# Kernel tuning notes

Measured on AMD Instinct MI355X. Metric: run time of the kernel, lower is better.

The kernel has to match this reference:

```python
import jax, jax.numpy as jnp
import numpy as np

H = 128  # hidden_dim

def setup_inputs() -> dict:
    key = jax.random.key(0)
    ks = jax.random.split(key, 8)
    B, S = 32, 512
    return {
        "CNN_output": jax.random.normal(ks[0], (B, 4 * S, H), jnp.float32),
        "gaz_input": jax.random.normal(ks[1], (B, S, 128), jnp.float32),
        "gaz_input_back": jax.random.normal(ks[2], (B, S, 128), jnp.float32),
        "global_matrix": jax.random.normal(ks[3], (B, S, H), jnp.float32),
        "exper_input": jax.random.normal(ks[4], (B, S, H), jnp.float32),
        "W_cat": jax.random.normal(ks[5], (3 * H, 16 * H), jnp.float32) * (1.0 / np.sqrt(3 * H)),
        "b_cat": jnp.zeros((16 * H,), jnp.float32),
        "W_exp": jax.random.normal(ks[6], (H, 12 * H), jnp.float32) * (1.0 / np.sqrt(H)),
        "b_exp": jnp.zeros((12 * H,), jnp.float32),
    }


def _diag_gather(y, B, S, width):
    # y: [B, 4*S, 4*width]; for seq-block j pick columns j*width:(j+1)*width
    y = y.reshape(B, 4, S, 4, width)
    j = jnp.arange(4)
    y = y[:, j, :, j, :]              # [4, B, S, width]
    return jnp.transpose(y, (1, 0, 2, 3)).reshape(B, 4 * S, width)


def reference(CNN_output, gaz_input, gaz_input_back, global_matrix, exper_input,
              W_cat, b_cat, W_exp, b_exp):
    B, S4, _ = CNN_output.shape
    S = S4 // 4
    gaz = jnp.concatenate([gaz_input, gaz_input_back, gaz_input, gaz_input_back], axis=1)
    gm = jnp.tile(global_matrix, (1, 4, 1))
    exp_rep = jnp.tile(exper_input, (1, 4, 1))
    cat_in = jnp.concatenate([CNN_output, gaz, gm], axis=2)      # [B, 4S, 3H]
    cat_gates = _diag_gather(cat_in @ W_cat + b_cat, B, S, 4 * H)  # [B, 4S, 4H]
    exper_gates = _diag_gather(exp_rep @ W_exp + b_exp, B, S, 3 * H)  # [B, 4S, 3H]
    new_state = jnp.tanh(cat_gates[:, :, :H])
    gates = jax.nn.sigmoid(cat_gates[:, :, H:] + exper_gates)
    gates = jax.nn.softmax(gates.reshape(B, S4, 3, H), axis=2)
    state_cat = jnp.stack([new_state, CNN_output, exp_rep], axis=2)  # [B, 4S, 3, H]
    layer_output = jnp.sum(gates * state_cat, axis=2)                # [B, 4S, H]
    return tuple(layer_output[:, i * S:(i + 1) * S] for i in range(4))
```

## Files before the change

kernel.cpp:

```cpp
#include <hip/hip_runtime.h>

typedef unsigned short u16;
typedef unsigned int u32;
typedef short bf16x8 __attribute__((ext_vector_type(8)));
typedef float f32x4 __attribute__((ext_vector_type(4)));

#define HH 128

__device__ __forceinline__ u16 f2bf(float f) {
  u32 u = __float_as_uint(f);
  u += 0x7fffu + ((u >> 16) & 1u);
  return (u16)(u >> 16);
}
__device__ __forceinline__ u32 pack2(float a, float b) {
  return (u32)f2bf(a) | ((u32)f2bf(b) << 16);
}

__device__ __forceinline__ void lds_dma16(const void* g, void* l) {
  __builtin_amdgcn_global_load_lds(
      (const __attribute__((address_space(1))) u32*)g,
      (__attribute__((address_space(3))) u32*)l, 16, 0, 0);
}

__global__ void prep_w(const float* __restrict__ Wcat,
                       const float* __restrict__ Wexp, u16* __restrict__ Wc) {
  int tid = blockIdx.x * 256 + threadIdx.x;
  int p = tid & 3;
  int n = (tid >> 2) & 511;
  int kc = (tid >> 11) & 15;
  int q = tid >> 15;
  int lq = p ^ (n & 3) ^ ((n >> 2) & 3);
  int k0 = kc * 32 + lq * 8;
  float v[8];
#pragma unroll
  for (int j = 0; j < 8; ++j) {
    int k = k0 + j;
    v[j] = (k < 384) ? Wcat[k * 2048 + q * 512 + n]
                     : ((n < 128) ? 0.f : Wexp[(k - 384) * 1536 + q * 384 + (n - 128)]);
  }
  uint4 pk;
  pk.x = pack2(v[0], v[1]);
  pk.y = pack2(v[2], v[3]);
  pk.z = pack2(v[4], v[5]);
  pk.w = pack2(v[6], v[7]);
  ((uint4*)Wc)[tid] = pk;
}

__global__ __launch_bounds__(256, 2) void fused_gate(
    const float* __restrict__ CNN, const float* __restrict__ gaz,
    const float* __restrict__ gazb, const float* __restrict__ gm,
    const float* __restrict__ exper, const u16* __restrict__ Wc,
    const float* __restrict__ bcat, const float* __restrict__ bexp,
    float* __restrict__ out) {
  __shared__ u16 Abuf[64 * 32];
  __shared__ u16 Wbuf[512 * 32];

  const int tid = threadIdx.x;
  const int bx = blockIdx.x;
  const int tile = bx & 7;
  const int grp = bx >> 3;
  const int b = grp >> 2;
  const int q = grp & 3;
  const int s_base = tile * 64;
  const int lane = tid & 63;
  const int wave = tid >> 6;
  const int l15 = lane & 15;
  const int quad = lane >> 4;
  const int physq = quad ^ (lane & 3) ^ ((lane >> 2) & 3);

  const int arow = tid >> 2;
  const int ap = tid & 3;
  const int alq = ap ^ (arow & 3) ^ ((arow >> 2) & 3);
  const int srow = s_base + arow;
  const float* s0 = CNN + (size_t)(b * 2048 + q * 512 + srow) * HH;
  const float* s1 = ((q & 1) ? gazb : gaz) + (size_t)(b * 512 + srow) * HH;
  const float* s2 = gm + (size_t)(b * 512 + srow) * HH;
  const float* s3 = exper + (size_t)(b * 512 + srow) * HH;

  const u16* wsrc = Wc + (size_t)q * 16 * 512 * 32;

  f32x4 acc[4][4][2];
#pragma unroll
  for (int rt = 0; rt < 4; ++rt)
#pragma unroll
    for (int gg = 0; gg < 4; ++gg)
#pragma unroll
      for (int u = 0; u < 2; ++u) acc[rt][gg][u] = (f32x4)0.f;

  for (int kc = 0; kc < 16; ++kc) {
    const int k0 = kc * 32 + alq * 8;
    const int sel = k0 >> 7;
    const float* sp = (sel == 0) ? s0 : (sel == 1) ? s1 : (sel == 2) ? s2 : s3;
    sp += (k0 & 127);
    float4 f0 = *(const float4*)sp;
    float4 f1 = *(const float4*)(sp + 4);
    uint4 pk;
    pk.x = pack2(f0.x, f0.y);
    pk.y = pack2(f0.z, f0.w);
    pk.z = pack2(f1.x, f1.y);
    pk.w = pack2(f1.z, f1.w);
    *(uint4*)&Abuf[arow * 32 + ap * 8] = pk;

    const u16* wchunk = wsrc + (size_t)kc * 512 * 32;
#pragma unroll
    for (int i = 0; i < 8; ++i)
      lds_dma16(wchunk + i * 2048 + wave * 512 + lane * 8,
                &Wbuf[i * 2048 + wave * 512]);
    __syncthreads();

    bf16x8 af[4];
#pragma unroll
    for (int rt = 0; rt < 4; ++rt)
      af[rt] = *(const bf16x8*)&Abuf[(rt * 16 + l15) * 32 + physq * 8];
    bf16x8 bfr[4][2];
#pragma unroll
    for (int gg = 0; gg < 4; ++gg)
#pragma unroll
      for (int u = 0; u < 2; ++u) {
        const int n = gg * 128 + wave * 32 + u * 16 + l15;
        bfr[gg][u] = *(const bf16x8*)&Wbuf[n * 32 + physq * 8];
      }
#pragma unroll
    for (int rt = 0; rt < 4; ++rt)
#pragma unroll
      for (int gg = 0; gg < 4; ++gg)
#pragma unroll
        for (int u = 0; u < 2; ++u)
          acc[rt][gg][u] = __builtin_amdgcn_mfma_f32_16x16x32_bf16(
              af[rt], bfr[gg][u], acc[rt][gg][u], 0, 0, 0);
    __syncthreads();
  }

  const float* bcq = bcat + q * 512;
  const float* beq = bexp + q * 384;
  const size_t cnnbase = (size_t)(b * 2048 + q * 512 + s_base) * HH;
  const size_t expbase = (size_t)(b * 512 + s_base) * HH;
  const size_t outbase = (size_t)((q * 32 + b) * 512 + s_base) * HH;
#pragma unroll
  for (int u = 0; u < 2; ++u) {
    const int h = wave * 32 + u * 16 + l15;
    const float bc0 = bcq[h];
    const float bc1 = bcq[128 + h];
    const float bc2 = bcq[256 + h];
    const float bc3 = bcq[384 + h];
    const float be1 = beq[h];
    const float be2 = beq[128 + h];
    const float be3 = beq[256 + h];
#pragma unroll
    for (int rt = 0; rt < 4; ++rt) {
#pragma unroll
      for (int r = 0; r < 4; ++r) {
        const int row = rt * 16 + quad * 4 + r;
        const float c0 = acc[rt][0][u][r] + bc0;
        const float p1 = acc[rt][1][u][r] + bc1 + be1;
        const float p2 = acc[rt][2][u][r] + bc2 + be2;
        const float p3 = acc[rt][3][u][r] + bc3 + be3;
        const float e2c = __expf(2.f * c0);
        const float ns = 1.f - 2.f * __builtin_amdgcn_rcpf(e2c + 1.f);
        const float g1 = __builtin_amdgcn_rcpf(1.f + __expf(-p1));
        const float g2 = __builtin_amdgcn_rcpf(1.f + __expf(-p2));
        const float g3 = __builtin_amdgcn_rcpf(1.f + __expf(-p3));
        const float e1 = __expf(g1);
        const float e2 = __expf(g2);
        const float e3 = __expf(g3);
        const float inv = __builtin_amdgcn_rcpf(e1 + e2 + e3);
        const float cnn = CNN[cnnbase + (size_t)row * HH + h];
        const float ex = exper[expbase + (size_t)row * HH + h];
        out[outbase + (size_t)row * HH + h] = (e1 * ns + e2 * cnn + e3 * ex) * inv;
      }
    }
  }
}

extern "C" void kernel_launch(void* const* d_in, const int* in_sizes, int n_in,
                              void* d_out, int out_size, void* d_ws, size_t ws_size,
                              hipStream_t stream) {
  const float* CNN = (const float*)d_in[0];
  const float* gaz = (const float*)d_in[1];
  const float* gazb = (const float*)d_in[2];
  const float* gm = (const float*)d_in[3];
  const float* exper = (const float*)d_in[4];
  const float* Wcat = (const float*)d_in[5];
  const float* bcat = (const float*)d_in[6];
  const float* Wexp = (const float*)d_in[7];
  const float* bexp = (const float*)d_in[8];
  u16* Wc = (u16*)d_ws;

  prep_w<<<512, 256, 0, stream>>>(Wcat, Wexp, Wc);
  fused_gate<<<1024, 256, 0, stream>>>(CNN, gaz, gazb, gm, exper, Wc, bcat,
                                       bexp, (float*)d_out);
}
```

Measured before the change: 168.8 us.

## Split gate GEMM across hidden halves and coalesce weight prep via LDS transpose

The fused gate kernel now splits each 64-row tile into two blocks, each covering half of the hidden columns. This halves the LDS weight buffer and the accumulator registers, doubles the grid, and raises the launch-bounds occupancy target from 2 to 3. The weight-prep kernel now reads rows with vectorized loads and transposes them through shared memory, replacing the earlier strided scalar gathers. The cost is that each activation tile is loaded and converted to bf16 twice, once per half.

New measurement: 174.8 us. +3.5%, slower.

```diff
diff --git a/kernel.cpp b/kernel.cpp
--- a/kernel.cpp
+++ b/kernel.cpp
@@ -22,51 +22,83 @@
       (__attribute__((address_space(3))) u32*)l, 16, 0, 0);
 }
 
-__global__ void prep_w(const float* __restrict__ Wcat,
-                       const float* __restrict__ Wexp, u16* __restrict__ Wc) {
-  int tid = blockIdx.x * 256 + threadIdx.x;
-  int p = tid & 3;
-  int n = (tid >> 2) & 511;
-  int kc = (tid >> 11) & 15;
-  int q = tid >> 15;
-  int lq = p ^ (n & 3) ^ ((n >> 2) & 3);
-  int k0 = kc * 32 + lq * 8;
+__global__ __launch_bounds__(256) void prep_w(const float* __restrict__ Wcat,
+                                              const float* __restrict__ Wexp,
+                                              u16* __restrict__ Wc) {
+  const int bx = blockIdx.x;
+  const int nt = bx & 7;
+  const int kc = (bx >> 3) & 15;
+  const int q = bx >> 7;
+  __shared__ u16 T[32 * 72];
+
+  const int tid = threadIdx.x;
+  const int r = tid >> 3;
+  const int c8 = (tid & 7) * 8;
   float v[8];
-#pragma unroll
-  for (int j = 0; j < 8; ++j) {
-    int k = k0 + j;
-    v[j] = (k < 384) ? Wcat[k * 2048 + q * 512 + n]
-                     : ((n < 128) ? 0.f : Wexp[(k - 384) * 1536 + q * 384 + (n - 128)]);
+  if (kc < 12) {
+    const float* src =
+        Wcat + (size_t)(kc * 32 + r) * 2048 + q * 512 + nt * 64 + c8;
+    float4 a = *(const float4*)src;
+    float4 b = *(const float4*)(src + 4);
+    v[0] = a.x; v[1] = a.y; v[2] = a.z; v[3] = a.w;
+    v[4] = b.x; v[5] = b.y; v[6] = b.z; v[7] = b.w;
+  } else if (nt >= 2) {
+    const float* src = Wexp + (size_t)((kc - 12) * 32 + r) * 1536 + q * 384 +
+                       nt * 64 + c8 - 128;
+    float4 a = *(const float4*)src;
+    float4 b = *(const float4*)(src + 4);
+    v[0] = a.x; v[1] = a.y; v[2] = a.z; v[3] = a.w;
+    v[4] = b.x; v[5] = b.y; v[6] = b.z; v[7] = b.w;
+  } else {
+#pragma unroll
+    for (int j = 0; j < 8; ++j) v[j] = 0.f;
   }
   uint4 pk;
   pk.x = pack2(v[0], v[1]);
   pk.y = pack2(v[2], v[3]);
   pk.z = pack2(v[4], v[5]);
   pk.w = pack2(v[6], v[7]);
-  ((uint4*)Wc)[tid] = pk;
-}
-
-__global__ __launch_bounds__(256, 2) void fused_gate(
+  *(uint4*)&T[r * 72 + c8] = pk;
+  __syncthreads();
+
+  const int p = tid & 3;
+  const int nl = tid >> 2;
+  const int lq = p ^ (nl & 3) ^ ((nl >> 2) & 3);
+  u16 w[8];
+#pragma unroll
+  for (int j = 0; j < 8; ++j) w[j] = T[(lq * 8 + j) * 72 + nl];
+  uint4 o;
+  o.x = (u32)w[0] | ((u32)w[1] << 16);
+  o.y = (u32)w[2] | ((u32)w[3] << 16);
+  o.z = (u32)w[4] | ((u32)w[5] << 16);
+  o.w = (u32)w[6] | ((u32)w[7] << 16);
+  const size_t idx = ((size_t)((q * 16 + kc) * 512) + nt * 64 + nl) * 4 + p;
+  ((uint4*)Wc)[idx] = o;
+}
+
+__global__ __launch_bounds__(256, 3) void fused_gate(
     const float* __restrict__ CNN, const float* __restrict__ gaz,
     const float* __restrict__ gazb, const float* __restrict__ gm,
     const float* __restrict__ exper, const u16* __restrict__ Wc,
     const float* __restrict__ bcat, const float* __restrict__ bexp,
     float* __restrict__ out) {
   __shared__ u16 Abuf[64 * 32];
-  __shared__ u16 Wbuf[512 * 32];
+  __shared__ u16 Wbuf[256 * 32];
 
   const int tid = threadIdx.x;
   const int bx = blockIdx.x;
-  const int tile = bx & 7;
-  const int grp = bx >> 3;
+  const int half = bx & 1;
+  const int tile = (bx >> 1) & 7;
+  const int grp = bx >> 4;
   const int b = grp >> 2;
   const int q = grp & 3;
   const int s_base = tile * 64;
+  const int h0 = half * 64;
   const int lane = tid & 63;
   const int wave = tid >> 6;
   const int l15 = lane & 15;
   const int quad = lane >> 4;
-  const int physq = quad ^ (lane & 3) ^ ((lane >> 2) & 3);
+  const int physq = quad ^ (l15 & 3) ^ ((l15 >> 2) & 3);
 
   const int arow = tid >> 2;
   const int ap = tid & 3;
@@ -79,13 +111,11 @@
 
   const u16* wsrc = Wc + (size_t)q * 16 * 512 * 32;
 
-  f32x4 acc[4][4][2];
+  f32x4 acc[4][4];
 #pragma unroll
   for (int rt = 0; rt < 4; ++rt)
 #pragma unroll
-    for (int gg = 0; gg < 4; ++gg)
-#pragma unroll
-      for (int u = 0; u < 2; ++u) acc[rt][gg][u] = (f32x4)0.f;
+    for (int gg = 0; gg < 4; ++gg) acc[rt][gg] = (f32x4)0.f;
 
   for (int kc = 0; kc < 16; ++kc) {
     const int k0 = kc * 32 + alq * 8;
@@ -103,31 +133,29 @@
 
     const u16* wchunk = wsrc + (size_t)kc * 512 * 32;
 #pragma unroll
-    for (int i = 0; i < 8; ++i)
-      lds_dma16(wchunk + i * 2048 + wave * 512 + lane * 8,
-                &Wbuf[i * 2048 + wave * 512]);
+    for (int i = 0; i < 4; ++i) {
+      const int n0 = wave * 128 + h0 + i * 16;
+      lds_dma16(wchunk + (size_t)n0 * 32 + lane * 8,
+                &Wbuf[(wave * 64 + i * 16) * 32]);
+    }
     __syncthreads();
 
     bf16x8 af[4];
 #pragma unroll
     for (int rt = 0; rt < 4; ++rt)
       af[rt] = *(const bf16x8*)&Abuf[(rt * 16 + l15) * 32 + physq * 8];
-    bf16x8 bfr[4][2];
-#pragma unroll
-    for (int gg = 0; gg < 4; ++gg)
-#pragma unroll
-      for (int u = 0; u < 2; ++u) {
-        const int n = gg * 128 + wave * 32 + u * 16 + l15;
-        bfr[gg][u] = *(const bf16x8*)&Wbuf[n * 32 + physq * 8];
-      }
+    bf16x8 bfr[4];
+#pragma unroll
+    for (int gg = 0; gg < 4; ++gg) {
+      const int c = gg * 64 + wave * 16 + l15;
+      bfr[gg] = *(const bf16x8*)&Wbuf[c * 32 + physq * 8];
+    }
 #pragma unroll
     for (int rt = 0; rt < 4; ++rt)
 #pragma unroll
       for (int gg = 0; gg < 4; ++gg)
-#pragma unroll
-        for (int u = 0; u < 2; ++u)
-          acc[rt][gg][u] = __builtin_amdgcn_mfma_f32_16x16x32_bf16(
-              af[rt], bfr[gg][u], acc[rt][gg][u], 0, 0, 0);
+        acc[rt][gg] = __builtin_amdgcn_mfma_f32_16x16x32_bf16(
+            af[rt], bfr[gg], acc[rt][gg], 0, 0, 0);
     __syncthreads();
   }
 
@@ -136,38 +164,35 @@
   const size_t cnnbase = (size_t)(b * 2048 + q * 512 + s_base) * HH;
   const size_t expbase = (size_t)(b * 512 + s_base) * HH;
   const size_t outbase = (size_t)((q * 32 + b) * 512 + s_base) * HH;
-#pragma unroll
-  for (int u = 0; u < 2; ++u) {
-    const int h = wave * 32 + u * 16 + l15;
-    const float bc0 = bcq[h];
-    const float bc1 = bcq[128 + h];
-    const float bc2 = bcq[256 + h];
-    const float bc3 = bcq[384 + h];
-    const float be1 = beq[h];
-    const float be2 = beq[128 + h];
-    const float be3 = beq[256 + h];
-#pragma unroll
-    for (int rt = 0; rt < 4; ++rt) {
-#pragma unroll
-      for (int r = 0; r < 4; ++r) {
-        const int row = rt * 16 + quad * 4 + r;
-        const float c0 = acc[rt][0][u][r] + bc0;
-        const float p1 = acc[rt][1][u][r] + bc1 + be1;
-        const float p2 = acc[rt][2][u][r] + bc2 + be2;
-        const float p3 = acc[rt][3][u][r] + bc3 + be3;
-        const float e2c = __expf(2.f * c0);
-        const float ns = 1.f - 2.f * __builtin_amdgcn_rcpf(e2c + 1.f);
-        const float g1 = __builtin_amdgcn_rcpf(1.f + __expf(-p1));
-        const float g2 = __builtin_amdgcn_rcpf(1.f + __expf(-p2));
-        const float g3 = __builtin_amdgcn_rcpf(1.f + __expf(-p3));
-        const float e1 = __expf(g1);
-        const float e2 = __expf(g2);
-        const float e3 = __expf(g3);
-        const float inv = __builtin_amdgcn_rcpf(e1 + e2 + e3);
-        const float cnn = CNN[cnnbase + (size_t)row * HH + h];
-        const float ex = exper[expbase + (size_t)row * HH + h];
-        out[outbase + (size_t)row * HH + h] = (e1 * ns + e2 * cnn + e3 * ex) * inv;
-      }
+  const int h = h0 + wave * 16 + l15;
+  const float bc0 = bcq[h];
+  const float bc1 = bcq[128 + h];
+  const float bc2 = bcq[256 + h];
+  const float bc3 = bcq[384 + h];
+  const float be1 = beq[h];
+  const float be2 = beq[128 + h];
+  const float be3 = beq[256 + h];
+#pragma unroll
+  for (int rt = 0; rt < 4; ++rt) {
+#pragma unroll
+    for (int r = 0; r < 4; ++r) {
+      const int row = rt * 16 + quad * 4 + r;
+      const float c0 = acc[rt][0][r] + bc0;
+      const float p1 = acc[rt][1][r] + bc1 + be1;
+      const float p2 = acc[rt][2][r] + bc2 + be2;
+      const float p3 = acc[rt][3][r] + bc3 + be3;
+      const float e2c = __expf(2.f * c0);
+      const float ns = 1.f - 2.f * __builtin_amdgcn_rcpf(e2c + 1.f);
+      const float g1 = __builtin_amdgcn_rcpf(1.f + __expf(-p1));
+      const float g2 = __builtin_amdgcn_rcpf(1.f + __expf(-p2));
+      const float g3 = __builtin_amdgcn_rcpf(1.f + __expf(-p3));
+      const float e1 = __expf(g1);
+      const float e2 = __expf(g2);
+      const float e3 = __expf(g3);
+      const float inv = __builtin_amdgcn_rcpf(e1 + e2 + e3);
+      const float cnn = CNN[cnnbase + (size_t)row * HH + h];
+      const float ex = exper[expbase + (size_t)row * HH + h];
+      out[outbase + (size_t)row * HH + h] = (e1 * ns + e2 * cnn + e3 * ex) * inv;
     }
   }
 }
@@ -187,6 +212,6 @@
   u16* Wc = (u16*)d_ws;
 
   prep_w<<<512, 256, 0, stream>>>(Wcat, Wexp, Wc);
-  fused_gate<<<1024, 256, 0, stream>>>(CNN, gaz, gazb, gm, exper, Wc, bcat,
+  fused_gate<<<2048, 256, 0, stream>>>(CNN, gaz, gazb, gm, exper, Wc, bcat,
                                        bexp, (float*)d_out);
 }
```
